# Optimization experiments

Hardware: AMD Instinct MI355X
Metric: run time of the kernel (lower is better)

## Reference

```python
import jax, jax.numpy as jnp
import numpy as np

H = 768          # hidden_size
HH = H // 2      # 384


def setup_inputs() -> dict:
    key = jax.random.key(0)
    ks = jax.random.split(key, 16)
    B, W, E, R = 32, 512, 128, 1024
    inp = {
        "hidden_states": jax.random.normal(ks[0], (B, W, H), dtype=jnp.float32),
        "relation_head": jax.random.randint(ks[1], (B, R), 0, E),
        "relation_tail": jax.random.randint(ks[2], (B, R), 0, E),
        "relation_label": jax.random.randint(ks[3], (B, R), 0, 2),
        "entities_start": jax.random.randint(ks[4], (B, E), 0, W),
        "entities_end": jax.random.randint(ks[5], (B, E), 0, W),
        "entities_label": jax.random.randint(ks[6], (B, E), 0, 3),
        # parameters (torch Linear convention: weight [out, in])
        "entity_emb": jax.random.normal(ks[7], (3, H), dtype=jnp.float32) * 0.02,
        "Wh1": jax.random.normal(ks[8], (H, 2 * H), dtype=jnp.float32) * 0.02,
        "bh1": jnp.zeros((H,), jnp.float32),
        "Wh2": jax.random.normal(ks[9], (HH, H), dtype=jnp.float32) * 0.02,
        "bh2": jnp.zeros((HH,), jnp.float32),
        "Wt1": jax.random.normal(ks[10], (H, 2 * H), dtype=jnp.float32) * 0.02,
        "bt1": jnp.zeros((H,), jnp.float32),
        "Wt2": jax.random.normal(ks[11], (HH, H), dtype=jnp.float32) * 0.02,
        "bt2": jnp.zeros((HH,), jnp.float32),
        "W_bil": jax.random.normal(ks[12], (2, HH, HH), dtype=jnp.float32) * 0.02,
        "W_lin": jax.random.normal(ks[13], (2, 2 * HH), dtype=jnp.float32) * 0.02,
        "b_lin": jnp.zeros((2,), jnp.float32),
    }
    return inp


def _ffnn(x, W1, b1, W2, b2):
    # two-layer MLP with ReLU (dropout is identity in eval mode)
    h = jax.nn.relu(jnp.einsum('brd,hd->brh', x, W1) + b1)
    return jax.nn.relu(jnp.einsum('brh,oh->bro', h, W2) + b2)


def reference(hidden_states, relation_head, relation_tail, relation_label,
              entities_start, entities_end, entities_label,
              entity_emb, Wh1, bh1, Wh2, bh2, Wt1, bt1, Wt2, bt2,
              W_bil, W_lin, b_lin):
    # gather per-relation entity info: [B, R]
    head_index = jnp.take_along_axis(entities_start, relation_head, axis=1)
    head_label = jnp.take_along_axis(entities_label, relation_head, axis=1)
    tail_index = jnp.take_along_axis(entities_start, relation_tail, axis=1)
    tail_label = jnp.take_along_axis(entities_label, relation_tail, axis=1)

    # gather token reprs: [B, R, H]
    head_tok = jnp.take_along_axis(hidden_states, head_index[:, :, None], axis=1)
    tail_tok = jnp.take_along_axis(hidden_states, tail_index[:, :, None], axis=1)

    head_repr = jnp.concatenate([head_tok, entity_emb[head_label]], axis=-1)  # [B,R,2H]
    tail_repr = jnp.concatenate([tail_tok, entity_emb[tail_label]], axis=-1)

    heads = _ffnn(head_repr, Wh1, bh1, Wh2, bh2)  # [B,R,HH]
    tails = _ffnn(tail_repr, Wt1, bt1, Wt2, bt2)

    # biaffine: bilinear + linear on concat
    bil = jnp.einsum('bri,oij,brj->bro', heads, W_bil, tails)
    lin = jnp.einsum('brc,oc->bro', jnp.concatenate([heads, tails], axis=-1), W_lin) + b_lin
    logits = bil + lin  # [B, R, 2]

    # per-doc mean CE summed over docs
    logp = jax.nn.log_softmax(logits, axis=-1)
    nll = -jnp.take_along_axis(logp, relation_label[:, :, None], axis=-1)[..., 0]  # [B,R]
    loss = jnp.sum(jnp.mean(nll, axis=1))
    return loss
```

## Files before the change

kernel.cpp:

```cpp
#include <hip/hip_runtime.h>
#include <math.h>

typedef unsigned short u16;
typedef __bf16 bf16x8 __attribute__((ext_vector_type(8)));
typedef float f32x4 __attribute__((ext_vector_type(4)));

#define B_ 32
#define W_ 512
#define H_ 768
#define HH_ 384
#define E_ 128
#define R_ 1024
#define BE_ 4096
#define K1_ 1536
#define BKK 64

__device__ __forceinline__ u16 f2bf(float f) {
  unsigned u = __float_as_uint(f);
  u = (u + 0x7fffu + ((u >> 16) & 1u)) >> 16;
  return (u16)u;
}
__device__ __forceinline__ float bf2f(u16 u) {
  return __uint_as_float(((unsigned)u) << 16);
}
__device__ __forceinline__ void gload_lds16(const void* g, void* l) {
  __builtin_amdgcn_global_load_lds(
      (__attribute__((address_space(1))) void*)(g),
      (__attribute__((address_space(3))) void*)(l), 16, 0, 0);
}

#define NBLK_W1 1152
#define NBLK_P  1152
#define NBLK_X  4096

__global__ __launch_bounds__(256) void prep_all(
    const float* __restrict__ Wh1, const float* __restrict__ Wt1,
    const float* __restrict__ bh1, const float* __restrict__ bt1,
    const float* __restrict__ emb,
    const float* __restrict__ hs, const int* __restrict__ ent_start,
    u16* __restrict__ W1c, float* __restrict__ P, u16* __restrict__ X)
{
  const int blk = blockIdx.x;
  const int tid = threadIdx.x;

  if (blk < NBLK_W1) {
    const int i = blk * 256 + tid;
    int row = i / 192, c = i % 192;
    const float4* src = (const float4*)((row < 768)
        ? (Wh1 + (size_t)row * K1_) : (Wt1 + (size_t)(row - 768) * K1_));
    float4 v = src[c];
    ushort4 o; o.x = f2bf(v.x); o.y = f2bf(v.y); o.z = f2bf(v.z); o.w = f2bf(v.w);
    ((ushort4*)W1c)[i] = o;
  } else if (blk < NBLK_W1 + NBLK_P) {
    const int w = (blk - NBLK_W1) * 4 + (tid >> 6);
    const int lane = tid & 63;
    const int l = w / K1_;
    const int n = w - l * K1_;
    const float* wrow = (n < 768) ? (Wh1 + (size_t)n * K1_ + 768)
                                  : (Wt1 + (size_t)(n - 768) * K1_ + 768);
    const float bb = (n < 768) ? bh1[n] : bt1[n - 768];
    const float* ev = emb + (size_t)l * H_;
    float s = 0.f;
#pragma unroll
    for (int t = 0; t < 12; ++t) {
      int d = lane + 64 * t;
      s += ev[d] * wrow[d];
    }
#pragma unroll
    for (int off = 32; off; off >>= 1) s += __shfl_down(s, off);
    if (lane == 0) P[(size_t)l * K1_ + n] = s + bb;
  } else {
    const int be = blk - (NBLK_W1 + NBLK_P);
    if (tid < 192) {
      int b = be >> 7;
      int start = ent_start[be];
      float4 v = ((const float4*)(hs + ((size_t)b * W_ + start) * H_))[tid];
      ushort4 o; o.x = f2bf(v.x); o.y = f2bf(v.y); o.z = f2bf(v.z); o.w = f2bf(v.w);
      ((ushort4*)(X + (size_t)be * H_))[tid] = o;
    }
  }
}

template<int TBM, int TBN>
__global__ __launch_bounds__(256, 2) void gemm_bf16(
    const u16* __restrict__ A, int lda,
    const u16* __restrict__ Wt,
    const float* __restrict__ bias,
    u16* __restrict__ C, int ldc,
    int K, int do_relu, int half_n, int aoff,
    const float* __restrict__ rowBias,
    const int* __restrict__ rowLabel, int ldP,
    int ngemm,
    const float* __restrict__ tWh2, const float* __restrict__ tWt2,
    const float* __restrict__ tWbil,
    const float* __restrict__ tbh2, const float* __restrict__ tbt2,
    u16* __restrict__ tW2c, u16* __restrict__ tWb, float* __restrict__ tb2cat,
    const u16* __restrict__ linSrc, const float* __restrict__ W_lin,
    float* __restrict__ linHT, float* __restrict__ outZ)
{
  constexpr int FM = TBM / 32;
  constexpr int FN = TBN / 32;
  constexpr int AU = TBM / 8;
  constexpr int UNITS = (TBM + TBN) / 8;
  constexpr int UPW = UNITS / 4;
  constexpr int BUFB = (TBM + TBN) * 128;

  __shared__ char smem[2 * BUFB];

  const int tid = threadIdx.x;
  const int id  = blockIdx.y * gridDim.x + blockIdx.x;

  if (id >= ngemm) {
    const int tailid = id - ngemm;
    const int ntail  = gridDim.x * gridDim.y - ngemm;
    if (tW2c) {
      for (int i = tailid * 256 + tid; i < 221376; i += ntail * 256) {
        if (i < 147456) {
          float4 v = (i < 73728) ? ((const float4*)tWh2)[i]
                                 : ((const float4*)tWt2)[i - 73728];
          ushort4 o; o.x = f2bf(v.x); o.y = f2bf(v.y); o.z = f2bf(v.z); o.w = f2bf(v.w);
          ((ushort4*)tW2c)[i] = o;
        } else if (i < 221184) {
          int j = i - 147456;
          float4 v = ((const float4*)tWbil)[j];
          ushort4 o; o.x = f2bf(v.x); o.y = f2bf(v.y); o.z = f2bf(v.z); o.w = f2bf(v.w);
          ((ushort4*)tWb)[j] = o;
        } else {
          int j = i - 221184;
          ((float4*)tb2cat)[j] = (j < 96) ? ((const float4*)tbh2)[j]
                                          : ((const float4*)tbt2)[j - 96];
        }
      }
    } else if (linHT) {
      if (tailid == 0 && tid == 0) outZ[0] = 0.f;
      const int wave  = tailid * 4 + (tid >> 6);
      const int nwave = ntail * 4;
      const int lane  = tid & 63;
      for (int be = wave; be < BE_; be += nwave) {
        const ushort4* src = (const ushort4*)(linSrc + (size_t)be * 768);
        float s0 = 0.f, s1 = 0.f, s2 = 0.f, s3 = 0.f;
#pragma unroll
        for (int rd = 0; rd < 3; ++rd) {
          const int idx4 = rd * 64 + lane;
          const int c = idx4 * 4;
          ushort4 v4 = src[idx4];
          float4 w0 = *(const float4*)(W_lin + c);
          float4 w1 = *(const float4*)(W_lin + 768 + c);
          float d0 = bf2f(v4.x)*w0.x + bf2f(v4.y)*w0.y + bf2f(v4.z)*w0.z + bf2f(v4.w)*w0.w;
          float d1 = bf2f(v4.x)*w1.x + bf2f(v4.y)*w1.y + bf2f(v4.z)*w1.z + bf2f(v4.w)*w1.w;
          if (c < 384) { s0 += d0; s1 += d1; }
          else         { s2 += d0; s3 += d1; }
        }
#pragma unroll
        for (int off = 32; off; off >>= 1) {
          s0 += __shfl_down(s0, off);
          s1 += __shfl_down(s1, off);
          s2 += __shfl_down(s2, off);
          s3 += __shfl_down(s3, off);
        }
        if (lane == 0) {
          float4 v = {s0, s1, s2, s3};
          *(float4*)(linHT + (size_t)be * 4) = v;
        }
      }
    }
    return;
  }

  const int q = ngemm >> 3, r = ngemm & 7;
  const int xcd = id & 7, idx = id >> 3;
  const int wgid = (xcd < r ? xcd * (q + 1) : r * (q + 1) + (xcd - r) * q) + idx;
  const int nbx = gridDim.x;
  const int bn = (wgid % nbx) * TBN;
  const int bm = (wgid / nbx) * TBM;

  const int wid  = tid >> 6;
  const int lane = tid & 63;
  const int wm = (wid >> 1) * (TBM / 2);
  const int wn = (wid & 1) * (TBN / 2);

  const int a0 = (half_n && bn >= half_n) ? aoff : 0;

  const int srow = lane >> 3;
  const int sk8  = (lane & 7) ^ srow;
  const u16* gA = A  + (size_t)(bm + srow) * lda + a0 + 8 * sk8;
  const u16* gB = Wt + (size_t)(bn + srow) * K + 8 * sk8;

  const int frow = lane & 15;
  const int fk8  = lane >> 4;

  f32x4 acc[FM][FN] = {};

  auto stage = [&](int buf, int k0) {
    char* base = smem + buf * BUFB;
#pragma unroll
    for (int i = 0; i < UPW; ++i) {
      const int u = wid * UPW + i;
      if (u < AU)
        gload_lds16(gA + (size_t)(u * 8) * lda + k0, base + u * 1024);
      else
        gload_lds16(gB + (size_t)((u - AU) * 8) * K + k0, base + u * 1024);
    }
  };

  const int nt = K / BKK;
  stage(0, 0);

  for (int t = 0; t < nt; ++t) {
    const int cur = t & 1;
    if (t + 1 < nt) {
      stage(cur ^ 1, (t + 1) * BKK);
      asm volatile("s_waitcnt vmcnt(%0)" :: "n"(UPW) : "memory");
    } else {
      asm volatile("s_waitcnt vmcnt(0)" ::: "memory");
    }
    __builtin_amdgcn_s_barrier();

    char* As = smem + cur * BUFB;
    char* Bs = As + TBM * 128;
#pragma unroll
    for (int kh = 0; kh < 2; ++kh) {
      bf16x8 a[FM], b[FN];
#pragma unroll
      for (int m = 0; m < FM; ++m) {
        const int row  = wm + m * 16 + frow;
        const int slot = (kh * 4 + fk8) ^ (row & 7);
        a[m] = *(const bf16x8*)(As + row * 128 + slot * 16);
      }
#pragma unroll
      for (int n = 0; n < FN; ++n) {
        const int row  = wn + n * 16 + frow;
        const int slot = (kh * 4 + fk8) ^ (row & 7);
        b[n] = *(const bf16x8*)(Bs + row * 128 + slot * 16);
      }
#pragma unroll
      for (int m = 0; m < FM; ++m)
#pragma unroll
        for (int n = 0; n < FN; ++n)
          acc[m][n] = __builtin_amdgcn_mfma_f32_16x16x32_bf16(
              a[m], b[n], acc[m][n], 0, 0, 0);
    }

    if (t + 1 < nt)
      __builtin_amdgcn_s_barrier();
  }

  int lbl[FM][4];
  if (rowLabel) {
#pragma unroll
    for (int m = 0; m < FM; ++m)
#pragma unroll
      for (int r2 = 0; r2 < 4; ++r2)
        lbl[m][r2] = rowLabel[bm + wm + m * 16 + fk8 * 4 + r2];
  }

#pragma unroll
  for (int n = 0; n < FN; ++n) {
    const int col = bn + wn + n * 16 + frow;
    const float bv = bias ? bias[col] : 0.f;
    float p0 = 0.f, p1 = 0.f, p2 = 0.f;
    if (rowLabel) {
      p0 = rowBias[col];
      p1 = rowBias[ldP + col];
      p2 = rowBias[2 * ldP + col];
    }
#pragma unroll
    for (int m = 0; m < FM; ++m) {
#pragma unroll
      for (int r2 = 0; r2 < 4; ++r2) {
        const int row = bm + wm + m * 16 + fk8 * 4 + r2;
        float v = acc[m][n][r2] + bv;
        if (rowLabel) {
          int l = lbl[m][r2];
          v += (l == 0) ? p0 : ((l == 1) ? p1 : p2);
        }
        if (do_relu) v = fmaxf(v, 0.f);
        C[(size_t)row * ldc + col] = f2bf(v);
      }
    }
  }
}

__global__ __launch_bounds__(256, 2) void gemm_S_ce(
    const u16* __restrict__ Hcat, const u16* __restrict__ U,
    const float* __restrict__ linHT, const float* __restrict__ b_lin,
    const int* __restrict__ rel_head, const int* __restrict__ rel_tail,
    const int* __restrict__ rel_label, float* __restrict__ out)
{
  __shared__ char smem[2 * 16384];
  __shared__ float Sl[64][65];
  __shared__ float red[4];

  const int xcd = blockIdx.x & 7, idx = blockIdx.x >> 3;
  const int wgid = xcd * 32 + idx;
  const int bn = (wgid & 3) * 64;
  const int zz = wgid >> 2;
  const int z  = zz >> 1;
  const int bm = (zz & 1) * 64;

  const int tid  = threadIdx.x;
  const int wid  = tid >> 6;
  const int lane = tid & 63;
  const int srow = lane >> 3;
  const int sk8  = (lane & 7) ^ srow;

  auto stage = [&](int buf, int k0) {
    char* base = smem + buf * 16384;
#pragma unroll
    for (int i = 0; i < 4; ++i) {
      const int u = wid * 4 + i;
      if (u < 8) {
        const int row = z*128 + bm + u*8 + srow;
        gload_lds16(Hcat + (size_t)row * 768 + k0 + 8*sk8, base + u*1024);
      } else {
        const int row = bn + (u - 8)*8 + srow;
        gload_lds16(U + (size_t)z*98304 + (size_t)row * 384 + k0 + 8*sk8,
                    base + u*1024);
      }
    }
  };

  const int wm = (wid >> 1) * 32;
  const int wn = (wid & 1) * 32;
  const int frow = lane & 15;
  const int fk8  = lane >> 4;

  f32x4 acc[2][2] = {};

  stage(0, 0);

  for (int t = 0; t < 6; ++t) {
    const int cur = t & 1;
    if (t + 1 < 6) {
      stage(cur ^ 1, (t + 1) * BKK);
      asm volatile("s_waitcnt vmcnt(4)" ::: "memory");
    } else {
      asm volatile("s_waitcnt vmcnt(0)" ::: "memory");
    }
    __builtin_amdgcn_s_barrier();

    char* As = smem + cur * 16384;
    char* Bs = As + 8192;
#pragma unroll
    for (int kh = 0; kh < 2; ++kh) {
      bf16x8 a[2], b[2];
#pragma unroll
      for (int m = 0; m < 2; ++m) {
        const int row  = wm + m*16 + frow;
        const int slot = (kh*4 + fk8) ^ (row & 7);
        a[m] = *(const bf16x8*)(As + row*128 + slot*16);
      }
#pragma unroll
      for (int n = 0; n < 2; ++n) {
        const int row  = wn + n*16 + frow;
        const int slot = (kh*4 + fk8) ^ (row & 7);
        b[n] = *(const bf16x8*)(Bs + row*128 + slot*16);
      }
#pragma unroll
      for (int m = 0; m < 2; ++m)
#pragma unroll
        for (int n = 0; n < 2; ++n)
          acc[m][n] = __builtin_amdgcn_mfma_f32_16x16x32_bf16(
              a[m], b[n], acc[m][n], 0, 0, 0);
    }

    if (t + 1 < 6)
      __builtin_amdgcn_s_barrier();
  }

  const int o = frow & 1;
  const float blv = b_lin[o];
#pragma unroll
  for (int n = 0; n < 2; ++n) {
    const int lc = wn + n*16 + frow;
    const int e2 = (bn + lc) >> 1;
    const float lt = linHT[(size_t)(z*128 + e2) * 4 + 2 + o];
#pragma unroll
    for (int m = 0; m < 2; ++m) {
#pragma unroll
      for (int r = 0; r < 4; ++r) {
        const int lr = wm + m*16 + fk8*4 + r;
        const float lh = linHT[(size_t)(z*128 + bm + lr) * 4 + o];
        Sl[lr][lc] = acc[m][n][r] + lh + lt + blv;
      }
    }
  }
  __syncthreads();

  float nllsum = 0.f;
#pragma unroll
  for (int j = 0; j < 4; ++j) {
    const int i = z * 1024 + tid + 256 * j;
    const int rh = rel_head[i];
    const int rt = rel_tail[i];
    const int lab = rel_label[i];
    if ((unsigned)(rh - bm) < 64u && (unsigned)(rt*2 - bn) < 64u) {
      const float l0 = Sl[rh - bm][rt*2 - bn];
      const float l1 = Sl[rh - bm][rt*2 - bn + 1];
      const float mx = fmaxf(l0, l1);
      const float lse = mx + logf(expf(l0 - mx) + expf(l1 - mx));
      nllsum += lse - (lab == 0 ? l0 : l1);
    }
  }
#pragma unroll
  for (int off = 32; off; off >>= 1) nllsum += __shfl_down(nllsum, off);
  if (lane == 0) red[wid] = nllsum;
  __syncthreads();
  if (tid == 0)
    atomicAdd(out, (red[0] + red[1] + red[2] + red[3]) * (1.0f / R_));
}

extern "C" void kernel_launch(void* const* d_in, const int* in_sizes, int n_in,
                              void* d_out, int out_size, void* d_ws, size_t ws_size,
                              hipStream_t stream)
{
  const float* hs        = (const float*)d_in[0];
  const int*   rel_head  = (const int*)  d_in[1];
  const int*   rel_tail  = (const int*)  d_in[2];
  const int*   rel_label = (const int*)  d_in[3];
  const int*   ent_start = (const int*)  d_in[4];
  const int*   ent_label = (const int*)  d_in[6];
  const float* emb   = (const float*)d_in[7];
  const float* Wh1   = (const float*)d_in[8];
  const float* bh1   = (const float*)d_in[9];
  const float* Wh2   = (const float*)d_in[10];
  const float* bh2   = (const float*)d_in[11];
  const float* Wt1   = (const float*)d_in[12];
  const float* bt1   = (const float*)d_in[13];
  const float* Wt2   = (const float*)d_in[14];
  const float* bt2   = (const float*)d_in[15];
  const float* Wbil  = (const float*)d_in[16];
  const float* W_lin = (const float*)d_in[17];
  const float* b_lin = (const float*)d_in[18];
  float* out = (float*)d_out;

  u16* X    = (u16*)d_ws;
  u16* H1   = X    + (size_t)BE_ * H_;
  u16* Hcat = H1   + (size_t)BE_ * K1_;
  u16* U    = Hcat + (size_t)BE_ * H_;
  u16* W1c  = U    + (size_t)BE_ * H_;
  u16* W2c  = W1c  + (size_t)K1_ * H_;
  u16* Wb   = W2c  + (size_t)H_ * H_;
  float* b2cat = (float*)(Wb + (size_t)H_ * HH_);
  float* P     = b2cat + H_;
  float* linHT = P + 3*K1_;

  prep_all<<<dim3(NBLK_W1 + NBLK_P + NBLK_X), dim3(256), 0, stream>>>(
      Wh1, Wt1, bh1, bt1, emb, hs, ent_start, W1c, P, X);

  gemm_bf16<128, 128><<<dim3(12, 34), dim3(256), 0, stream>>>(
      X, H_, W1c, (const float*)nullptr, H1, K1_, H_, 1, 0, 0,
      P, ent_label, K1_, 384,
      Wh2, Wt2, Wbil, bh2, bt2, W2c, Wb, b2cat,
      (const u16*)nullptr, (const float*)nullptr, (float*)nullptr, (float*)nullptr);

  gemm_bf16<128, 96><<<dim3(8, 32), dim3(256), 0, stream>>>(
      H1, K1_, W2c, b2cat, Hcat, H_, H_, 1, HH_, H_,
      (const float*)nullptr, (const int*)nullptr, 0, 256,
      (const float*)nullptr, (const float*)nullptr, (const float*)nullptr,
      (const float*)nullptr, (const float*)nullptr,
      (u16*)nullptr, (u16*)nullptr, (float*)nullptr,
      (const u16*)nullptr, (const float*)nullptr, (float*)nullptr, (float*)nullptr);

  gemm_bf16<128, 96><<<dim3(8, 49), dim3(256), 0, stream>>>(
      Hcat + HH_, H_, Wb, (const float*)nullptr, U, H_, HH_, 0, 0, 0,
      (const float*)nullptr, (const int*)nullptr, 0, 256,
      (const float*)nullptr, (const float*)nullptr, (const float*)nullptr,
      (const float*)nullptr, (const float*)nullptr,
      (u16*)nullptr, (u16*)nullptr, (float*)nullptr,
      Hcat, W_lin, linHT, out);

  gemm_S_ce<<<dim3(256), dim3(256), 0, stream>>>(
      Hcat, U, linHT, b_lin, rel_head, rel_tail, rel_label, out);
}
```

Before: 61.10 us.

## Add triple-buffered LDS pipeline to second GEMM and S kernel, batch gather rows

Makes the GEMM pipeline depth a template parameter and uses a three-stage LDS buffer, prefetching two K-tiles ahead, for the second FFNN GEMM (with min-blocks lowered to 1) and for the bilinear/CE kernel. In the CE kernel the logits scratch now reuses the staging shared memory instead of a separate array. The gather/convert part of the prep kernel handles eight entity rows per block, so it launches far fewer blocks. The aim is to hide global-load latency and cut block-launch overhead, at the cost of more LDS per block and possibly lower occupancy.

Result: no change. 61.15 us (+0.1%).

```diff
diff --git a/kernel.cpp b/kernel.cpp
--- a/kernel.cpp
+++ b/kernel.cpp
@@ -31,7 +31,7 @@
 
 #define NBLK_W1 1152
 #define NBLK_P  1152
-#define NBLK_X  4096
+#define NBLK_X  512
 
 __global__ __launch_bounds__(256) void prep_all(
     const float* __restrict__ Wh1, const float* __restrict__ Wt1,
@@ -70,19 +70,23 @@
     for (int off = 32; off; off >>= 1) s += __shfl_down(s, off);
     if (lane == 0) P[(size_t)l * K1_ + n] = s + bb;
   } else {
-    const int be = blk - (NBLK_W1 + NBLK_P);
+    const int g = blk - (NBLK_W1 + NBLK_P);
     if (tid < 192) {
-      int b = be >> 7;
-      int start = ent_start[be];
-      float4 v = ((const float4*)(hs + ((size_t)b * W_ + start) * H_))[tid];
-      ushort4 o; o.x = f2bf(v.x); o.y = f2bf(v.y); o.z = f2bf(v.z); o.w = f2bf(v.w);
-      ((ushort4*)(X + (size_t)be * H_))[tid] = o;
-    }
-  }
-}
-
-template<int TBM, int TBN>
-__global__ __launch_bounds__(256, 2) void gemm_bf16(
+#pragma unroll
+      for (int e = 0; e < 8; ++e) {
+        const int be = g * 8 + e;
+        int b = be >> 7;
+        int start = ent_start[be];
+        float4 v = ((const float4*)(hs + ((size_t)b * W_ + start) * H_))[tid];
+        ushort4 o; o.x = f2bf(v.x); o.y = f2bf(v.y); o.z = f2bf(v.z); o.w = f2bf(v.w);
+        ((ushort4*)(X + (size_t)be * H_))[tid] = o;
+      }
+    }
+  }
+}
+
+template<int TBM, int TBN, int DEPTH, int MINB>
+__global__ __launch_bounds__(256, MINB) void gemm_bf16(
     const u16* __restrict__ A, int lda,
     const u16* __restrict__ Wt,
     const float* __restrict__ bias,
@@ -105,7 +109,7 @@
   constexpr int UPW = UNITS / 4;
   constexpr int BUFB = (TBM + TBN) * 128;
 
-  __shared__ char smem[2 * BUFB];
+  __shared__ char smem[DEPTH * BUFB];
 
   const int tid = threadIdx.x;
   const int id  = blockIdx.y * gridDim.x + blockIdx.x;
@@ -205,14 +209,26 @@
 
   const int nt = K / BKK;
   stage(0, 0);
+  if (DEPTH == 3 && nt > 1) stage(1, BKK);
 
   for (int t = 0; t < nt; ++t) {
-    const int cur = t & 1;
-    if (t + 1 < nt) {
-      stage(cur ^ 1, (t + 1) * BKK);
-      asm volatile("s_waitcnt vmcnt(%0)" :: "n"(UPW) : "memory");
+    const int cur = t % DEPTH;
+    if (DEPTH == 2) {
+      if (t + 1 < nt) {
+        stage((t + 1) % DEPTH, (t + 1) * BKK);
+        asm volatile("s_waitcnt vmcnt(%0)" :: "n"(UPW) : "memory");
+      } else {
+        asm volatile("s_waitcnt vmcnt(0)" ::: "memory");
+      }
     } else {
-      asm volatile("s_waitcnt vmcnt(0)" ::: "memory");
+      if (t + 2 < nt) {
+        stage((t + 2) % DEPTH, (t + 2) * BKK);
+        asm volatile("s_waitcnt vmcnt(%0)" :: "n"(2 * UPW) : "memory");
+      } else if (t + 1 < nt) {
+        asm volatile("s_waitcnt vmcnt(%0)" :: "n"(UPW) : "memory");
+      } else {
+        asm volatile("s_waitcnt vmcnt(0)" ::: "memory");
+      }
     }
     __builtin_amdgcn_s_barrier();
 
@@ -287,9 +303,9 @@
     const int* __restrict__ rel_head, const int* __restrict__ rel_tail,
     const int* __restrict__ rel_label, float* __restrict__ out)
 {
-  __shared__ char smem[2 * 16384];
-  __shared__ float Sl[64][65];
-  __shared__ float red[4];
+  __shared__ char smem[3 * 16384];
+  float* Sl  = (float*)smem;
+  float* red = (float*)(smem + 64 * 65 * 4);
 
   const int xcd = blockIdx.x & 7, idx = blockIdx.x >> 3;
   const int wgid = xcd * 32 + idx;
@@ -328,11 +344,14 @@
   f32x4 acc[2][2] = {};
 
   stage(0, 0);
+  stage(1, BKK);
 
   for (int t = 0; t < 6; ++t) {
-    const int cur = t & 1;
-    if (t + 1 < 6) {
-      stage(cur ^ 1, (t + 1) * BKK);
+    const int cur = t % 3;
+    if (t + 2 < 6) {
+      stage((t + 2) % 3, (t + 2) * BKK);
+      asm volatile("s_waitcnt vmcnt(8)" ::: "memory");
+    } else if (t + 1 < 6) {
       asm volatile("s_waitcnt vmcnt(4)" ::: "memory");
     } else {
       asm volatile("s_waitcnt vmcnt(0)" ::: "memory");
@@ -381,7 +400,7 @@
       for (int r = 0; r < 4; ++r) {
         const int lr = wm + m*16 + fk8*4 + r;
         const float lh = linHT[(size_t)(z*128 + bm + lr) * 4 + o];
-        Sl[lr][lc] = acc[m][n][r] + lh + lt + blv;
+        Sl[lr * 65 + lc] = acc[m][n][r] + lh + lt + blv;
       }
     }
   }
@@ -395,8 +414,8 @@
     const int rt = rel_tail[i];
     const int lab = rel_label[i];
     if ((unsigned)(rh - bm) < 64u && (unsigned)(rt*2 - bn) < 64u) {
-      const float l0 = Sl[rh - bm][rt*2 - bn];
-      const float l1 = Sl[rh - bm][rt*2 - bn + 1];
+      const float l0 = Sl[(rh - bm) * 65 + (rt*2 - bn)];
+      const float l1 = Sl[(rh - bm) * 65 + (rt*2 - bn) + 1];
       const float mx = fmaxf(l0, l1);
       const float lse = mx + logf(expf(l0 - mx) + expf(l1 - mx));
       nllsum += lse - (lab == 0 ? l0 : l1);
@@ -448,13 +467,13 @@
   prep_all<<<dim3(NBLK_W1 + NBLK_P + NBLK_X), dim3(256), 0, stream>>>(
       Wh1, Wt1, bh1, bt1, emb, hs, ent_start, W1c, P, X);
 
-  gemm_bf16<128, 128><<<dim3(12, 34), dim3(256), 0, stream>>>(
+  gemm_bf16<128, 128, 2, 2><<<dim3(12, 34), dim3(256), 0, stream>>>(
       X, H_, W1c, (const float*)nullptr, H1, K1_, H_, 1, 0, 0,
       P, ent_label, K1_, 384,
       Wh2, Wt2, Wbil, bh2, bt2, W2c, Wb, b2cat,
       (const u16*)nullptr, (const float*)nullptr, (float*)nullptr, (float*)nullptr);
 
-  gemm_bf16<128, 96><<<dim3(8, 32), dim3(256), 0, stream>>>(
+  gemm_bf16<128, 96, 3, 1><<<dim3(8, 32), dim3(256), 0, stream>>>(
       H1, K1_, W2c, b2cat, Hcat, H_, H_, 1, HH_, H_,
       (const float*)nullptr, (const int*)nullptr, 0, 256,
       (const float*)nullptr, (const float*)nullptr, (const float*)nullptr,
@@ -462,7 +481,7 @@
       (u16*)nullptr, (u16*)nullptr, (float*)nullptr,
       (const u16*)nullptr, (const float*)nullptr, (float*)nullptr, (float*)nullptr);
 
-  gemm_bf16<128, 96><<<dim3(8, 49), dim3(256), 0, stream>>>(
+  gemm_bf16<128, 96, 2, 2><<<dim3(8, 49), dim3(256), 0, stream>>>(
       Hcat + HH_, H_, Wb, (const float*)nullptr, U, H_, HH_, 0, 0, 0,
       (const float*)nullptr, (const int*)nullptr, 0, 256,
       (const float*)nullptr, (const float*)nullptr, (const float*)nullptr,
```
